# Optimization experiments

Hardware: AMD Instinct MI355X
Metric: run time of the kernel (lower is better)

The kernel has to match this reference:

```python
import jax, jax.numpy as jnp
import numpy as np

V_WORD = 32000      # word vocab (dictionary.symbols minus specials)
NGRAM_VOCAB = 32001 # threshold top ngrams + UNK
DIM = 128
LATENT = 10000
NSPECIAL = 4
PAD_IDX = 1         # fairseq pad index
NG_PER_WORD = 26    # avg char-ngrams per word for n=4
B, T = 8, 1024


def setup_inputs() -> dict:
    key = jax.random.key(0)
    k1, k2, k3, k4, k5 = jax.random.split(key, 5)
    ngram_emb_weight = jax.random.normal(k1, (NGRAM_VOCAB, DIM), jnp.float32) * (DIM ** -0.5)
    latent_mat = jax.random.normal(k2, (LATENT, DIM), jnp.float32) * (LATENT ** -0.5)
    special_emb = jax.random.normal(k3, (NSPECIAL, DIM), jnp.float32) * (DIM ** -0.5)
    special_emb = special_emb.at[PAD_IDX].set(0.0)  # nn.init.constant_(special_emb[pad], 0)
    ngram_ids = jax.random.randint(k4, (V_WORD * NG_PER_WORD,), 0, NGRAM_VOCAB, jnp.int32)
    ngram_offsets = jnp.arange(V_WORD, dtype=jnp.int32) * NG_PER_WORD
    x = jax.random.randint(k5, (B, T), 0, NSPECIAL + V_WORD, jnp.int32)
    return {
        "ngram_emb_weight": ngram_emb_weight,
        "latent_mat": latent_mat,
        "special_emb": special_emb,
        "ngram_ids": ngram_ids,
        "ngram_offsets": ngram_offsets,
        "x": x,
    }


def reference(ngram_emb_weight, latent_mat, special_emb, ngram_ids, ngram_offsets, x):
    n_total = ngram_ids.shape[0]
    # EmbeddingBag(mode='sum'): segment-sum gathered ngram vectors per word
    seg = jnp.searchsorted(ngram_offsets, jnp.arange(n_total, dtype=ngram_offsets.dtype), side='right') - 1
    bag = jax.ops.segment_sum(ngram_emb_weight[ngram_ids], seg, num_segments=V_WORD)  # [V_WORD, DIM]
    lang_emb = jnp.tanh(bag)
    # softmax attention over the latent codebook
    latent_scores = jnp.einsum('vd,ld->vl', lang_emb, latent_mat)          # [V_WORD, LATENT]
    latent_distribution = jax.nn.softmax(latent_scores, axis=-1)
    latent_emb = jnp.einsum('vl,ld->vd', latent_distribution, latent_mat)  # [V_WORD, DIM]
    token_emb = lang_emb + latent_emb
    emb_weight = jnp.concatenate([special_emb, token_emb], axis=0)          # [NSPECIAL+V_WORD, DIM]
    sde_emb = emb_weight[x]                                                 # [B, T, DIM]
    return sde_emb
```

## Files before the change

### kernel.cpp

```cpp
#include <hip/hip_runtime.h>

typedef float  f32x4 __attribute__((ext_vector_type(4)));
typedef short  s16x8 __attribute__((ext_vector_type(8)));
typedef int    i32x4 __attribute__((ext_vector_type(4)));
typedef unsigned short u16x4 __attribute__((ext_vector_type(4)));
typedef unsigned int   u32x2 __attribute__((ext_vector_type(2)));

#define V_WORD   32000
#define DIM      128
#define LATENT   10000
#define NSPECIAL 4
#define NTOK     8192
#define NTILE    157
#define BN       64

__device__ __forceinline__ unsigned short f2bf(float f) {
  unsigned u = __builtin_bit_cast(unsigned, f);
  unsigned r = (u + 0x7fffu + ((u >> 16) & 1u)) >> 16;
  return (unsigned short)r;
}

__device__ __forceinline__ unsigned cvt_pk_bf16(float lo, float hi) {
  unsigned r;
  asm("v_cvt_pk_bf16_f32 %0, %1, %2" : "=v"(r) : "v"(lo), "v"(hi));
  return r;
}

__global__ __launch_bounds__(256) void k0_convert(
    const float* __restrict__ latent, unsigned short* __restrict__ Lb,
    unsigned short* __restrict__ LTb) {
  __shared__ float tile[64][129];
  int l0 = blockIdx.x * 64;
  int r  = threadIdx.x >> 2;
  int c0 = (threadIdx.x & 3) * 32;
  int l  = l0 + r;
  for (int k = 0; k < 8; ++k) {
    int d = c0 + k * 4;
    f32x4 v = {0.f, 0.f, 0.f, 0.f};
    if (l < LATENT) v = *reinterpret_cast<const f32x4*>(latent + (size_t)l * DIM + d);
    tile[r][d + 0] = v[0]; tile[r][d + 1] = v[1];
    tile[r][d + 2] = v[2]; tile[r][d + 3] = v[3];
    if (l < LATENT) {
      u16x4 o = { f2bf(v[0]), f2bf(v[1]), f2bf(v[2]), f2bf(v[3]) };
      *reinterpret_cast<u16x4*>(Lb + (size_t)l * DIM + d) = o;
    }
  }
  __syncthreads();
  int d = threadIdx.x >> 1;
  int lbase = (threadIdx.x & 1) * 32;
  for (int k = 0; k < 16; ++k) {
    int ll = lbase + 2 * k;
    int l1 = l0 + ll;
    if (l1 + 1 < LATENT) {
      unsigned pack = (unsigned)f2bf(tile[ll][d]) | ((unsigned)f2bf(tile[ll + 1][d]) << 16);
      *reinterpret_cast<unsigned*>(LTb + (size_t)d * LATENT + l1) = pack;
    } else if (l1 < LATENT) {
      LTb[(size_t)d * LATENT + l1] = f2bf(tile[ll][d]);
    }
  }
}

__global__ __launch_bounds__(256) void k1_bag(
    const float* __restrict__ ngram_emb, const int* __restrict__ ids,
    const int* __restrict__ offs, const int* __restrict__ x,
    float* __restrict__ langf, unsigned short* __restrict__ langb) {
  int tok  = blockIdx.x * 4 + (threadIdx.x >> 6);
  int lane = threadIdx.x & 63;
  int half = lane >> 5;
  int l32  = lane & 31;
  int w = x[tok];
  f32x4 s0 = {0.f, 0.f, 0.f, 0.f}, s1 = {0.f, 0.f, 0.f, 0.f};
  if (w >= NSPECIAL) {
    int base = offs[w - NSPECIAL];
#pragma unroll
    for (int j = 0; j < 24; j += 4) {
      int ia = ids[base + j + half];
      int ib = ids[base + j + 2 + half];
      s0 += *reinterpret_cast<const f32x4*>(ngram_emb + (size_t)ia * DIM + l32 * 4);
      s1 += *reinterpret_cast<const f32x4*>(ngram_emb + (size_t)ib * DIM + l32 * 4);
    }
    int ic = ids[base + 24 + half];
    s0 += *reinterpret_cast<const f32x4*>(ngram_emb + (size_t)ic * DIM + l32 * 4);
    s0 += s1;
    for (int c = 0; c < 4; ++c) s0[c] += __shfl_xor(s0[c], 32, 64);
    for (int c = 0; c < 4; ++c) s0[c] = tanhf(s0[c]);
  }
  if (half == 0) {
    *reinterpret_cast<f32x4*>(langf + (size_t)tok * DIM + l32 * 4) = s0;
  } else {
    u32x2 pw = { cvt_pk_bf16(s0[0], s0[1]), cvt_pk_bf16(s0[2], s0[3]) };
    *reinterpret_cast<u32x2*>(langb + (size_t)tok * DIM + l32 * 4) = pw;
  }
}

__global__ __launch_bounds__(256, 2) void k2_fused(
    const unsigned short* __restrict__ Lb,
    const unsigned short* __restrict__ LTb,
    const unsigned short* __restrict__ langb,
    float* __restrict__ Opart,
    float* __restrict__ Zpart,
    int nsplit) {
  __shared__ alignas(16) unsigned short Lsh[64 * DIM];
  __shared__ alignas(16) unsigned short LTsh[DIM * 64];
  __shared__ alignas(16) unsigned short Psh[128 * 64];
  __shared__ float zsh[128];

  int bid = blockIdx.x;
  int xcd = bid & 7, idx = bid >> 3;
  int split, tokblk;
  if (nsplit == 8)      { split = xcd;                   tokblk = idx; }
  else if (nsplit == 16){ split = xcd * 2 + (idx >> 6);  tokblk = idx & 63; }
  else                  { split = xcd >> 1;              tokblk = idx + ((xcd & 1) << 5); }
  int tokbase = tokblk * 128;
  int t0 = (split * NTILE) / nsplit, t1 = ((split + 1) * NTILE) / nsplit;
  int lat_s = t0 * BN;
  int lat_e = min(t1 * BN, LATENT);
  int ntiles = t1 - t0;
  int npad = t1 * BN - lat_e;

  int tid = threadIdx.x;
  int wid = tid >> 6, lane = tid & 63;
  int lr = lane & 15, lg = lane >> 4;
  int wm = wid & 1, wn = wid >> 1;

  int rL  = tid >> 4, csL = tid & 15;
  int coL = csL ^ (rL & 7);
  int ddT = tid >> 3, csT = tid & 7;
  int coT = csT ^ (ddT & 7);

  s16x8 Bl[4][4];
  for (int n = 0; n < 4; ++n) {
    int row = tokbase + wn * 64 + n * 16 + lr;
    for (int kf = 0; kf < 4; ++kf)
      Bl[n][kf] = *reinterpret_cast<const s16x8*>(langb + (size_t)row * DIM + (kf * 4 + lg) * 8);
  }

  f32x4 acc2[4][4];
  for (int a = 0; a < 4; ++a)
    for (int b = 0; b < 4; ++b) acc2[a][b] = {0.f, 0.f, 0.f, 0.f};
  float zp[4] = {0.f, 0.f, 0.f, 0.f};

  i32x4 stgL[4], stgT[4];
  auto prefetch = [&](int t) {
    int lat0 = lat_s + t * BN;
#pragma unroll
    for (int i = 0; i < 4; ++i) {
      int r = rL + i * 16;
      i32x4 v = {0, 0, 0, 0};
      if (lat0 + r < lat_e)
        v = *reinterpret_cast<const i32x4*>(Lb + (size_t)(lat0 + r) * DIM + coL * 8);
      stgL[i] = v;
    }
    bool okT = (lat0 + coT * 8 + 8 <= lat_e);
#pragma unroll
    for (int i = 0; i < 4; ++i) {
      int dd = ddT + i * 32;
      i32x4 v = {0, 0, 0, 0};
      if (okT)
        v = *reinterpret_cast<const i32x4*>(LTb + (size_t)dd * LATENT + lat0 + coT * 8);
      stgT[i] = v;
    }
  };

  prefetch(0);

  for (int t = 0; t < ntiles; ++t) {
#pragma unroll
    for (int i = 0; i < 4; ++i)
      *reinterpret_cast<i32x4*>(&Lsh[(rL + i * 16) * DIM + csL * 8]) = stgL[i];
#pragma unroll
    for (int i = 0; i < 4; ++i)
      *reinterpret_cast<i32x4*>(&LTsh[(ddT + i * 32) * 64 + csT * 8]) = stgT[i];
    __syncthreads();

    if (t + 1 < ntiles) prefetch(t + 1);

    f32x4 acc1[2][4];
    for (int m = 0; m < 2; ++m)
      for (int n = 0; n < 4; ++n) acc1[m][n] = {0.f, 0.f, 0.f, 0.f};
    for (int kf = 0; kf < 4; ++kf) {
      s16x8 a[2];
      for (int m = 0; m < 2; ++m) {
        int row = wm * 32 + m * 16 + lr;
        int c = kf * 4 + lg;
        a[m] = *reinterpret_cast<const s16x8*>(&Lsh[row * DIM + (c ^ (row & 7)) * 8]);
      }
      __builtin_amdgcn_s_setprio(1);
      for (int m = 0; m < 2; ++m)
        for (int n = 0; n < 4; ++n)
          acc1[m][n] = __builtin_amdgcn_mfma_f32_16x16x32_bf16(a[m], Bl[n][kf], acc1[m][n], 0, 0, 0);
      __builtin_amdgcn_s_setprio(0);
    }

    for (int m = 0; m < 2; ++m) {
      int la0 = wm * 32 + m * 16 + lg * 4;
      for (int n = 0; n < 4; ++n) {
        f32x4 v = acc1[m][n];
        float p0 = __expf(v[0]), p1 = __expf(v[1]);
        float p2 = __expf(v[2]), p3 = __expf(v[3]);
        zp[n] += p0; zp[n] += p1; zp[n] += p2; zp[n] += p3;
        u32x2 pw = { cvt_pk_bf16(p0, p1), cvt_pk_bf16(p2, p3) };
        int row = wn * 64 + n * 16 + lr;
        int c = la0 >> 3;
        *reinterpret_cast<u32x2*>(&Psh[row * 64 + ((c ^ (row & 7)) << 3) + (la0 & 7)]) = pw;
      }
    }
    __syncthreads();

    for (int kf = 0; kf < 2; ++kf) {
      s16x8 Ap[4], Bt[4];
      int c = kf * 4 + lg;
      for (int mr = 0; mr < 4; ++mr) {
        int row = wm * 64 + mr * 16 + lr;
        Ap[mr] = *reinterpret_cast<const s16x8*>(&Psh[row * 64 + ((c ^ (row & 7)) << 3)]);
      }
      for (int nd = 0; nd < 4; ++nd) {
        int dr = wn * 64 + nd * 16 + lr;
        Bt[nd] = *reinterpret_cast<const s16x8*>(&LTsh[dr * 64 + ((c ^ (dr & 7)) << 3)]);
      }
      __builtin_amdgcn_s_setprio(1);
      for (int mr = 0; mr < 4; ++mr)
        for (int nd = 0; nd < 4; ++nd)
          acc2[mr][nd] = __builtin_amdgcn_mfma_f32_16x16x32_bf16(Ap[mr], Bt[nd], acc2[mr][nd], 0, 0, 0);
      __builtin_amdgcn_s_setprio(0);
    }
    __syncthreads();
  }

  for (int n = 0; n < 4; ++n) {
    zp[n] += __shfl_xor(zp[n], 16, 64);
    zp[n] += __shfl_xor(zp[n], 32, 64);
  }
  if (wm == 0 && lane < 16)
    for (int n = 0; n < 4; ++n) zsh[wn * 64 + n * 16 + lr] = zp[n];
  __syncthreads();
  if (wm == 1 && lane < 16)
    for (int n = 0; n < 4; ++n) zsh[wn * 64 + n * 16 + lr] += zp[n];
  __syncthreads();

  for (int mr = 0; mr < 4; ++mr) {
    int rbase = wm * 64 + mr * 16 + lg * 4;
    for (int nd = 0; nd < 4; ++nd) {
      int dcol = wn * 64 + nd * 16 + lr;
      for (int i = 0; i < 4; ++i) {
        int row = rbase + i;
        Opart[((size_t)split * NTOK + tokbase + row) * DIM + dcol] = acc2[mr][nd][i];
      }
    }
  }
  if (tid < 128)
    Zpart[split * NTOK + tokbase + tid] = zsh[tid] - (float)npad;
}

__global__ __launch_bounds__(256) void k3_combine(
    const float* __restrict__ special, const int* __restrict__ x,
    const float* __restrict__ langf, const float* __restrict__ Opart,
    const float* __restrict__ Zpart, float* __restrict__ out, int nsplit) {
  int gi  = blockIdx.x * 256 + threadIdx.x;
  int tok = gi >> 5;
  int d4  = (gi & 31) * 4;
  int w   = x[tok];
  f32x4 o;
  if (w < NSPECIAL) {
    o = *reinterpret_cast<const f32x4*>(special + (size_t)w * DIM + d4);
  } else {
    f32x4 s = {0.f, 0.f, 0.f, 0.f};
    float z = 0.f;
    for (int sp = 0; sp < nsplit; ++sp) {
      s += *reinterpret_cast<const f32x4*>(Opart + ((size_t)sp * NTOK + tok) * DIM + d4);
      z += Zpart[sp * NTOK + tok];
    }
    f32x4 lg = *reinterpret_cast<const f32x4*>(langf + (size_t)tok * DIM + d4);
    o = lg + s / z;
  }
  *reinterpret_cast<f32x4*>(out + (size_t)tok * DIM + d4) = o;
}

extern "C" void kernel_launch(void* const* d_in, const int* in_sizes, int n_in,
                              void* d_out, int out_size, void* d_ws, size_t ws_size,
                              hipStream_t stream) {
  const float* ngram_emb = (const float*)d_in[0];
  const float* latent    = (const float*)d_in[1];
  const float* special   = (const float*)d_in[2];
  const int*   ids       = (const int*)d_in[3];
  const int*   offs      = (const int*)d_in[4];
  const int*   x         = (const int*)d_in[5];
  float* out = (float*)d_out;

  size_t fixed = (size_t)LATENT * DIM * 2 * 2
               + (size_t)NTOK * DIM * 4
               + (size_t)NTOK * DIM * 2;
  int nsplit = 8;
  while (nsplit > 4) {
    size_t need = fixed + (size_t)nsplit * NTOK * DIM * 4 + (size_t)nsplit * NTOK * 4;
    if (need <= ws_size) break;
    nsplit >>= 1;
  }

  char* w = (char*)d_ws;
  unsigned short* Lb  = (unsigned short*)w;  w += (size_t)LATENT * DIM * 2;
  unsigned short* LTb = (unsigned short*)w;  w += (size_t)DIM * LATENT * 2;
  float* langf        = (float*)w;           w += (size_t)NTOK * DIM * 4;
  unsigned short* langb = (unsigned short*)w; w += (size_t)NTOK * DIM * 2;
  float* Opart        = (float*)w;           w += (size_t)nsplit * NTOK * DIM * 4;
  float* Zpart        = (float*)w;           w += (size_t)nsplit * NTOK * 4;

  hipLaunchKernelGGL(k0_convert, dim3((LATENT + 63) / 64), dim3(256), 0, stream,
                     latent, Lb, LTb);
  hipLaunchKernelGGL(k1_bag, dim3(NTOK / 4), dim3(256), 0, stream,
                     ngram_emb, ids, offs, x, langf, langb);
  hipLaunchKernelGGL(k2_fused, dim3(nsplit * 64), dim3(256), 0, stream,
                     Lb, LTb, langb, Opart, Zpart, nsplit);
  hipLaunchKernelGGL(k3_combine, dim3(NTOK * DIM / 4 / 256), dim3(256), 0, stream,
                     special, x, langf, Opart, Zpart, out, nsplit);
}
```

Measured before the change: 157.9 us.

## Merge latent convert and bag kernels, use fast tanh, raise split count and occupancy

Folds the latent bf16 conversion/transposition and the ngram bag-sum into one launch, so a single grid of 32-row convert blocks plus bag blocks runs back to back without a kernel boundary. Replaces tanhf with an exp/reciprocal approximation. Raises the default latent split from 8 to 16 when the workspace allows it, and bumps k2 launch bounds to 3 blocks per CU. The trade-offs are more partial-output traffic for the combine step, possible register spilling under the tighter bound, and slightly different tanh accuracy.

```diff
diff --git a/kernel.cpp b/kernel.cpp
--- a/kernel.cpp
+++ b/kernel.cpp
@@ -13,6 +13,7 @@
 #define NTOK     8192
 #define NTILE    157
 #define BN       64
+#define K0_BLOCKS 313
 
 __device__ __forceinline__ unsigned short f2bf(float f) {
   unsigned u = __builtin_bit_cast(unsigned, f);
@@ -26,74 +27,79 @@
   return r;
 }
 
-__global__ __launch_bounds__(256) void k0_convert(
+__device__ __forceinline__ float tanh_fast(float x) {
+  float t = __expf(2.f * x);
+  return (t - 1.f) * __frcp_rn(t + 1.f);
+}
+
+__global__ __launch_bounds__(256) void k01_prep(
     const float* __restrict__ latent, unsigned short* __restrict__ Lb,
-    unsigned short* __restrict__ LTb) {
-  __shared__ float tile[64][129];
-  int l0 = blockIdx.x * 64;
-  int r  = threadIdx.x >> 2;
-  int c0 = (threadIdx.x & 3) * 32;
-  int l  = l0 + r;
-  for (int k = 0; k < 8; ++k) {
-    int d = c0 + k * 4;
-    f32x4 v = {0.f, 0.f, 0.f, 0.f};
-    if (l < LATENT) v = *reinterpret_cast<const f32x4*>(latent + (size_t)l * DIM + d);
-    tile[r][d + 0] = v[0]; tile[r][d + 1] = v[1];
-    tile[r][d + 2] = v[2]; tile[r][d + 3] = v[3];
-    if (l < LATENT) {
-      u16x4 o = { f2bf(v[0]), f2bf(v[1]), f2bf(v[2]), f2bf(v[3]) };
-      *reinterpret_cast<u16x4*>(Lb + (size_t)l * DIM + d) = o;
-    }
-  }
-  __syncthreads();
-  int d = threadIdx.x >> 1;
-  int lbase = (threadIdx.x & 1) * 32;
-  for (int k = 0; k < 16; ++k) {
-    int ll = lbase + 2 * k;
-    int l1 = l0 + ll;
-    if (l1 + 1 < LATENT) {
-      unsigned pack = (unsigned)f2bf(tile[ll][d]) | ((unsigned)f2bf(tile[ll + 1][d]) << 16);
-      *reinterpret_cast<unsigned*>(LTb + (size_t)d * LATENT + l1) = pack;
-    } else if (l1 < LATENT) {
-      LTb[(size_t)d * LATENT + l1] = f2bf(tile[ll][d]);
-    }
-  }
-}
-
-__global__ __launch_bounds__(256) void k1_bag(
+    unsigned short* __restrict__ LTb,
     const float* __restrict__ ngram_emb, const int* __restrict__ ids,
     const int* __restrict__ offs, const int* __restrict__ x,
     float* __restrict__ langf, unsigned short* __restrict__ langb) {
-  int tok  = blockIdx.x * 4 + (threadIdx.x >> 6);
-  int lane = threadIdx.x & 63;
-  int half = lane >> 5;
-  int l32  = lane & 31;
-  int w = x[tok];
-  f32x4 s0 = {0.f, 0.f, 0.f, 0.f}, s1 = {0.f, 0.f, 0.f, 0.f};
-  if (w >= NSPECIAL) {
-    int base = offs[w - NSPECIAL];
-#pragma unroll
-    for (int j = 0; j < 24; j += 4) {
-      int ia = ids[base + j + half];
-      int ib = ids[base + j + 2 + half];
-      s0 += *reinterpret_cast<const f32x4*>(ngram_emb + (size_t)ia * DIM + l32 * 4);
-      s1 += *reinterpret_cast<const f32x4*>(ngram_emb + (size_t)ib * DIM + l32 * 4);
-    }
-    int ic = ids[base + 24 + half];
-    s0 += *reinterpret_cast<const f32x4*>(ngram_emb + (size_t)ic * DIM + l32 * 4);
-    s0 += s1;
-    for (int c = 0; c < 4; ++c) s0[c] += __shfl_xor(s0[c], 32, 64);
-    for (int c = 0; c < 4; ++c) s0[c] = tanhf(s0[c]);
-  }
-  if (half == 0) {
-    *reinterpret_cast<f32x4*>(langf + (size_t)tok * DIM + l32 * 4) = s0;
+  __shared__ float tile[32][129];
+  int bid = blockIdx.x;
+  int tid = threadIdx.x;
+  if (bid < K0_BLOCKS) {
+    int l0 = bid * 32;
+    int r  = tid >> 3;
+    int c0 = (tid & 7) * 16;
+    int l  = l0 + r;
+    for (int k = 0; k < 4; ++k) {
+      int d = c0 + k * 4;
+      f32x4 v = {0.f, 0.f, 0.f, 0.f};
+      if (l < LATENT) v = *reinterpret_cast<const f32x4*>(latent + (size_t)l * DIM + d);
+      tile[r][d + 0] = v[0]; tile[r][d + 1] = v[1];
+      tile[r][d + 2] = v[2]; tile[r][d + 3] = v[3];
+      if (l < LATENT) {
+        u16x4 o = { f2bf(v[0]), f2bf(v[1]), f2bf(v[2]), f2bf(v[3]) };
+        *reinterpret_cast<u16x4*>(Lb + (size_t)l * DIM + d) = o;
+      }
+    }
+    __syncthreads();
+    int d = tid >> 1;
+    int lbase = (tid & 1) * 16;
+    for (int k = 0; k < 8; ++k) {
+      int ll = lbase + 2 * k;
+      int l1 = l0 + ll;
+      if (l1 < LATENT) {
+        unsigned pack = (unsigned)f2bf(tile[ll][d]) | ((unsigned)f2bf(tile[ll + 1][d]) << 16);
+        *reinterpret_cast<unsigned*>(LTb + (size_t)d * LATENT + l1) = pack;
+      }
+    }
   } else {
-    u32x2 pw = { cvt_pk_bf16(s0[0], s0[1]), cvt_pk_bf16(s0[2], s0[3]) };
-    *reinterpret_cast<u32x2*>(langb + (size_t)tok * DIM + l32 * 4) = pw;
-  }
-}
-
-__global__ __launch_bounds__(256, 2) void k2_fused(
+    int tok  = (bid - K0_BLOCKS) * 4 + (tid >> 6);
+    int lane = tid & 63;
+    int half = lane >> 5;
+    int l32  = lane & 31;
+    int w = x[tok];
+    f32x4 s0 = {0.f, 0.f, 0.f, 0.f}, s1 = {0.f, 0.f, 0.f, 0.f};
+    if (w >= NSPECIAL) {
+      int base = offs[w - NSPECIAL];
+#pragma unroll
+      for (int j = 0; j < 24; j += 4) {
+        int ia = ids[base + j + half];
+        int ib = ids[base + j + 2 + half];
+        s0 += *reinterpret_cast<const f32x4*>(ngram_emb + (size_t)ia * DIM + l32 * 4);
+        s1 += *reinterpret_cast<const f32x4*>(ngram_emb + (size_t)ib * DIM + l32 * 4);
+      }
+      int ic = ids[base + 24 + half];
+      s0 += *reinterpret_cast<const f32x4*>(ngram_emb + (size_t)ic * DIM + l32 * 4);
+      s0 += s1;
+      for (int c = 0; c < 4; ++c) s0[c] += __shfl_xor(s0[c], 32, 64);
+      for (int c = 0; c < 4; ++c) s0[c] = tanh_fast(s0[c]);
+    }
+    if (half == 0) {
+      *reinterpret_cast<f32x4*>(langf + (size_t)tok * DIM + l32 * 4) = s0;
+    } else {
+      u32x2 pw = { cvt_pk_bf16(s0[0], s0[1]), cvt_pk_bf16(s0[2], s0[3]) };
+      *reinterpret_cast<u32x2*>(langb + (size_t)tok * DIM + l32 * 4) = pw;
+    }
+  }
+}
+
+__global__ __launch_bounds__(256, 3) void k2_fused(
     const unsigned short* __restrict__ Lb,
     const unsigned short* __restrict__ LTb,
     const unsigned short* __restrict__ langb,
@@ -108,8 +114,8 @@
   int bid = blockIdx.x;
   int xcd = bid & 7, idx = bid >> 3;
   int split, tokblk;
-  if (nsplit == 8)      { split = xcd;                   tokblk = idx; }
-  else if (nsplit == 16){ split = xcd * 2 + (idx >> 6);  tokblk = idx & 63; }
+  if (nsplit == 16)     { split = xcd * 2 + (idx >> 6);  tokblk = idx & 63; }
+  else if (nsplit == 8) { split = xcd;                   tokblk = idx; }
   else                  { split = xcd >> 1;              tokblk = idx + ((xcd & 1) << 5); }
   int tokbase = tokblk * 128;
   int t0 = (split * NTILE) / nsplit, t1 = ((split + 1) * NTILE) / nsplit;
@@ -290,7 +296,7 @@
   size_t fixed = (size_t)LATENT * DIM * 2 * 2
                + (size_t)NTOK * DIM * 4
                + (size_t)NTOK * DIM * 2;
-  int nsplit = 8;
+  int nsplit = 16;
   while (nsplit > 4) {
     size_t need = fixed + (size_t)nsplit * NTOK * DIM * 4 + (size_t)nsplit * NTOK * 4;
     if (need <= ws_size) break;
@@ -305,10 +311,8 @@
   float* Opart        = (float*)w;           w += (size_t)nsplit * NTOK * DIM * 4;
   float* Zpart        = (float*)w;           w += (size_t)nsplit * NTOK * 4;
 
-  hipLaunchKernelGGL(k0_convert, dim3((LATENT + 63) / 64), dim3(256), 0, stream,
-                     latent, Lb, LTb);
-  hipLaunchKernelGGL(k1_bag, dim3(NTOK / 4), dim3(256), 0, stream,
-                     ngram_emb, ids, offs, x, langf, langb);
+  hipLaunchKernelGGL(k01_prep, dim3(K0_BLOCKS + NTOK / 4), dim3(256), 0, stream,
+                     latent, Lb, LTb, ngram_emb, ids, offs, x, langf, langb);
   hipLaunchKernelGGL(k2_fused, dim3(nsplit * 64), dim3(256), 0, stream,
                      Lb, LTb, langb, Opart, Zpart, nsplit);
   hipLaunchKernelGGL(k3_combine, dim3(NTOK * DIM / 4 / 256), dim3(256), 0, stream,
```

Result: slower. 287.2 us (+81.9%).
